# Optimization experiments

Hardware: AMD Instinct MI355X
Metric: run time of the kernel (lower is better)

## Reference

```python
import jax, jax.numpy as jnp
import numpy as np

N_CLASSES = 256
PER_CLASS = 128
N_SUPPORT = 5
N_QUERY = PER_CLASS - N_SUPPORT  # 123
N_VIEW = 2
D = 384
N = N_CLASSES * PER_CLASS  # 32768


def setup_inputs() -> dict:
    key = jax.random.key(0)
    k1, k2 = jax.random.split(key, 2)
    reps = jax.random.normal(k1, (N, N_VIEW, D), dtype=jnp.float32)
    # block-sorted labels: class c occupies rows [c*PER_CLASS, (c+1)*PER_CLASS)
    labels = (jnp.arange(N, dtype=jnp.int32) // PER_CLASS).astype(jnp.int32)
    return {"reps": reps, "labels": labels}


def reference(reps, labels):
    # labels are block-sorted per class, so the original's
    # labels.eq(c).nonzero()[:n_support] / [n_support:] gathers are static reshapes.
    reps_r = reps.reshape(N_CLASSES, PER_CLASS, N_VIEW, D)
    # class-mean prototypes over the support set: [C, V, D]
    prototypes = reps_r[:, :N_SUPPORT].mean(axis=1)
    # query samples: [C*N_QUERY, V, D]
    queries = reps_r[:, N_SUPPORT:].reshape(N_CLASSES * N_QUERY, N_VIEW, D)

    x2 = jnp.sum(queries * queries, axis=-1)            # [n, V]
    y2 = jnp.sum(prototypes * prototypes, axis=-1)      # [m, V]
    xy = jnp.einsum('nvd,mvd->nmv', queries, prototypes)  # [n, m, V]
    dists = x2[:, None, :] + y2[None, :, :] - 2.0 * xy

    # log_softmax over the prototype (class) axis
    log_p_y = jax.nn.log_softmax(-dists, axis=1)
    log_p_y = log_p_y.reshape(N_CLASSES, N_QUERY, N_CLASSES, N_VIEW)

    # gather the true-class log-prob for each query / view
    cls = jnp.arange(N_CLASSES)
    correct = log_p_y[cls, :, cls, :]  # [C, N_QUERY, V]
    loss = -correct.mean()
    return loss
```

## Files before the change

### kernel.cpp

```cpp
#include <hip/hip_runtime.h>
#include <hip/hip_bf16.h>
#include <math.h>

#define NCLS 256
#define PER_CLASS 128
#define NSUP 5
#define NQRY 123
#define NVIEW 2
#define DD 384
#define NQ_TOT (NCLS * NQRY)
#define BM 128
#define BK 32
#define QSTR 40
#define PSTR 40

#define PROTO_F (NVIEW * NCLS * DD)

typedef __attribute__((ext_vector_type(8))) short short8;
typedef __attribute__((ext_vector_type(4))) float floatx4;

union FragU { uint4 u; short8 s; };
union PkU { __hip_bfloat162 b2; unsigned int u; };

__device__ __forceinline__ unsigned int cvt2bf(float lo, float hi) {
    PkU p;
    p.b2 = __float22bfloat162_rn(make_float2(lo, hi));
    return p.u;
}

__global__ __launch_bounds__(256) void proto_kernel(const float* __restrict__ reps,
                                                    float* __restrict__ protof,
                                                    ushort* __restrict__ pbf) {
    int g = blockIdx.x * 256 + threadIdx.x;
    int d = g % DD;
    int rest = g / DD;
    int c = rest & (NCLS - 1);
    int v = rest >> 8;
    const float* p = reps + ((size_t)(c * PER_CLASS) * NVIEW + v) * DD + d;
    float s = 0.f;
#pragma unroll
    for (int k = 0; k < NSUP; ++k) s += p[(size_t)k * NVIEW * DD];
    s *= 0.2f;
    protof[g] = s;
    __hip_bfloat16 h = __float2bfloat16(s);
    pbf[g] = *reinterpret_cast<ushort*>(&h);
}

__global__ __launch_bounds__(64) void y2_kernel(const float* __restrict__ protof,
                                                float* __restrict__ y2) {
    int b = blockIdx.x;
    int lane = threadIdx.x;
    const float* p = protof + (size_t)b * DD;
    float s = 0.f;
#pragma unroll
    for (int k = 0; k < DD / 64; ++k) { float x = p[lane + 64 * k]; s += x * x; }
#pragma unroll
    for (int o = 1; o < 64; o <<= 1) s += __shfl_xor(s, o);
    if (lane == 0) y2[b] = s;
}

__global__ __launch_bounds__(256, 2) void main_kernel(const float* __restrict__ reps,
                                                      const ushort* __restrict__ pbf,
                                                      const float* __restrict__ y2g,
                                                      float* __restrict__ out) {
    __shared__ ushort q_lds[BM * QSTR];
    __shared__ ushort p_lds[NCLS * PSTR];
    __shared__ float pmx[BM][2];
    __shared__ float pse[BM][2];
    __shared__ float wred[8];

    const int t = threadIdx.x;
    const int v = blockIdx.y;
    const int q0 = blockIdx.x * BM;
    const int wave = t >> 6;
    const int lane = t & 63;
    const int col = lane & 15;
    const int quad = lane >> 4;
    const int wm = wave >> 1;
    const int wn = wave & 1;

    const int sqrow = t >> 1;
    const int sqh = (t & 1) * 16;
    const int nq = q0 + sqrow;
    const float* qsrc = reps +
        (size_t)((nq / NQRY) * PER_CLASS + NSUP + (nq % NQRY)) * (NVIEW * DD) + v * DD + sqh;
    const ushort* psrc = pbf + (size_t)(v * NCLS + t) * DD;

    floatx4 acc[4][8];
#pragma unroll
    for (int mt = 0; mt < 4; ++mt)
#pragma unroll
        for (int nt = 0; nt < 8; ++nt) acc[mt][nt] = (floatx4)0.f;

    for (int kt = 0; kt < DD / BK; ++kt) {
        float4 qf0 = *(const float4*)(qsrc + kt * BK);
        float4 qf1 = *(const float4*)(qsrc + kt * BK + 4);
        float4 qf2 = *(const float4*)(qsrc + kt * BK + 8);
        float4 qf3 = *(const float4*)(qsrc + kt * BK + 12);
        const uint4* pp = (const uint4*)(psrc + kt * BK);
        uint4 pl0 = pp[0], pl1 = pp[1], pl2 = pp[2], pl3 = pp[3];

        if (kt) __syncthreads();

        uint4 qw0, qw1;
        qw0.x = cvt2bf(qf0.x, qf0.y); qw0.y = cvt2bf(qf0.z, qf0.w);
        qw0.z = cvt2bf(qf1.x, qf1.y); qw0.w = cvt2bf(qf1.z, qf1.w);
        qw1.x = cvt2bf(qf2.x, qf2.y); qw1.y = cvt2bf(qf2.z, qf2.w);
        qw1.z = cvt2bf(qf3.x, qf3.y); qw1.w = cvt2bf(qf3.z, qf3.w);
        *(uint4*)&q_lds[sqrow * QSTR + sqh] = qw0;
        *(uint4*)&q_lds[sqrow * QSTR + sqh + 8] = qw1;
        *(uint4*)&p_lds[t * PSTR + 0] = pl0;
        *(uint4*)&p_lds[t * PSTR + 8] = pl1;
        *(uint4*)&p_lds[t * PSTR + 16] = pl2;
        *(uint4*)&p_lds[t * PSTR + 24] = pl3;
        __syncthreads();

        short8 af[4];
#pragma unroll
        for (int mt = 0; mt < 4; ++mt) {
            FragU f;
            f.u = *(const uint4*)&q_lds[(wm * 64 + mt * 16 + col) * QSTR + quad * 8];
            af[mt] = f.s;
        }
#pragma unroll
        for (int nt = 0; nt < 8; ++nt) {
            FragU b;
            b.u = *(const uint4*)&p_lds[(wn * 128 + nt * 16 + col) * PSTR + quad * 8];
#pragma unroll
            for (int mt = 0; mt < 4; ++mt)
                acc[mt][nt] = __builtin_amdgcn_mfma_f32_16x16x32_bf16(af[mt], b.s, acc[mt][nt], 0, 0, 0);
        }
    }

    float y2c[8];
#pragma unroll
    for (int nt = 0; nt < 8; ++nt) y2c[nt] = y2g[v * NCLS + wn * 128 + nt * 16 + col];

    float corr = 0.f;
#pragma unroll
    for (int mt = 0; mt < 4; ++mt) {
#pragma unroll
        for (int r = 0; r < 4; ++r) {
            const int qloc = wm * 64 + mt * 16 + quad * 4 + r;
            const int n = q0 + qloc;
            const int cn = n / NQRY;
            float s[8];
            float mx = -1e30f;
#pragma unroll
            for (int nt = 0; nt < 8; ++nt) {
                s[nt] = 2.f * acc[mt][nt][r] - y2c[nt];
                mx = fmaxf(mx, s[nt]);
                if (cn == wn * 128 + nt * 16 + col) corr += s[nt];
            }
#pragma unroll
            for (int o = 1; o < 16; o <<= 1) mx = fmaxf(mx, __shfl_xor(mx, o));
            float e = 0.f;
#pragma unroll
            for (int nt = 0; nt < 8; ++nt) e += __expf(s[nt] - mx);
#pragma unroll
            for (int o = 1; o < 16; o <<= 1) e += __shfl_xor(e, o);
            if (col == 0) { pmx[qloc][wn] = mx; pse[qloc][wn] = e; }
        }
    }
#pragma unroll
    for (int o = 1; o < 64; o <<= 1) corr += __shfl_xor(corr, o);
    if (lane == 0) wred[wave] = corr;
    __syncthreads();

    float lval = 0.f;
    if (t < BM) {
        float m0 = pmx[t][0], m1 = pmx[t][1];
        float M = fmaxf(m0, m1);
        float E = pse[t][0] * __expf(m0 - M) + pse[t][1] * __expf(m1 - M);
        lval = M + __logf(E);
    }
#pragma unroll
    for (int o = 1; o < 64; o <<= 1) lval += __shfl_xor(lval, o);
    if (lane == 0) wred[4 + wave] = lval;
    __syncthreads();

    if (t == 0) {
        float tot = (wred[4] + wred[5] + wred[6] + wred[7]) -
                    (wred[0] + wred[1] + wred[2] + wred[3]);
        atomicAdd(out, tot * (1.f / (float)(NQ_TOT * NVIEW)));
    }
}

extern "C" void kernel_launch(void* const* d_in, const int* in_sizes, int n_in,
                              void* d_out, int out_size, void* d_ws, size_t ws_size,
                              hipStream_t stream) {
    const float* reps = (const float*)d_in[0];
    float* ws = (float*)d_ws;
    float* protof = ws;
    float* y2 = ws + PROTO_F;
    ushort* pbf = (ushort*)(ws + PROTO_F + 512);
    float* out = (float*)d_out;

    hipMemsetAsync(out, 0, sizeof(float), stream);
    proto_kernel<<<dim3(PROTO_F / 256), dim3(256), 0, stream>>>(reps, protof, pbf);
    y2_kernel<<<dim3(NVIEW * NCLS), dim3(64), 0, stream>>>(protof, y2);
    main_kernel<<<dim3(NQ_TOT / BM, NVIEW), dim3(256), 0, stream>>>(reps, pbf, y2, out);
}
```

Measured before the change: 169.0 us.

## Load tiles directly to LDS via global_load_lds with XOR-swizzled layout

Replaces the register-staged global->LDS copies with direct global_load_lds 16-byte transfers for both query (fp32) and prototype (bf16) tiles. It uses XOR swizzles instead of row padding to avoid bank conflicts. The fp32->bf16 conversion of queries moves from the staging step to fragment load time, so each wave converts its own A fragments. This cuts register pressure and VALU staging work but doubles the LDS footprint for query tiles. It also drops the software overlap where global loads were issued before the barrier.

```diff
diff --git a/kernel.cpp b/kernel.cpp
--- a/kernel.cpp
+++ b/kernel.cpp
@@ -11,8 +11,6 @@
 #define NQ_TOT (NCLS * NQRY)
 #define BM 128
 #define BK 32
-#define QSTR 40
-#define PSTR 40
 
 #define PROTO_F (NVIEW * NCLS * DD)
 
@@ -26,6 +24,12 @@
     PkU p;
     p.b2 = __float22bfloat162_rn(make_float2(lo, hi));
     return p.u;
+}
+
+__device__ __forceinline__ void load16(const void* g, void* l) {
+    __builtin_amdgcn_global_load_lds(
+        (const __attribute__((address_space(1))) unsigned int*)g,
+        (__attribute__((address_space(3))) unsigned int*)l, 16, 0, 0);
 }
 
 __global__ __launch_bounds__(256) void proto_kernel(const float* __restrict__ reps,
@@ -63,8 +67,8 @@
                                                       const ushort* __restrict__ pbf,
                                                       const float* __restrict__ y2g,
                                                       float* __restrict__ out) {
-    __shared__ ushort q_lds[BM * QSTR];
-    __shared__ ushort p_lds[NCLS * PSTR];
+    __shared__ float q_lds[BM * BK];
+    __shared__ ushort p_lds[NCLS * BK];
     __shared__ float pmx[BM][2];
     __shared__ float pse[BM][2];
     __shared__ float wred[8];
@@ -79,12 +83,25 @@
     const int wm = wave >> 1;
     const int wn = wave & 1;
 
-    const int sqrow = t >> 1;
-    const int sqh = (t & 1) * 16;
-    const int nq = q0 + sqrow;
-    const float* qsrc = reps +
-        (size_t)((nq / NQRY) * PER_CLASS + NSUP + (nq % NQRY)) * (NVIEW * DD) + v * DD + sqh;
-    const ushort* psrc = pbf + (size_t)(v * NCLS + t) * DD;
+    const int l8 = lane >> 3, c8 = lane & 7;
+    const int cdq = c8 ^ l8;
+    const int l4 = lane >> 2;
+    const int cdp = (lane & 3) ^ ((lane >> 3) & 3);
+    const float* qptr[4];
+    const ushort* pptr[4];
+#pragma unroll
+    for (int i = 0; i < 4; ++i) {
+        int r = wave * 32 + i * 8 + l8;
+        int nq = q0 + r;
+        qptr[i] = reps + (size_t)((nq / NQRY) * PER_CLASS + NSUP + (nq % NQRY)) * (NVIEW * DD) +
+                  v * DD + cdq * 4;
+        int pr = wave * 64 + i * 16 + l4;
+        pptr[i] = pbf + (size_t)(v * NCLS + pr) * DD + cdp * 8;
+    }
+
+    const float* abase0 = q_lds + (wm * 64 + col) * 32 + ((2 * quad + 0) ^ (col & 7)) * 4;
+    const float* abase1 = q_lds + (wm * 64 + col) * 32 + ((2 * quad + 1) ^ (col & 7)) * 4;
+    const ushort* bbase = p_lds + (wn * 128 + col) * 32 + (quad ^ ((col >> 1) & 3)) * 8;
 
     floatx4 acc[4][8];
 #pragma unroll
@@ -93,39 +110,30 @@
         for (int nt = 0; nt < 8; ++nt) acc[mt][nt] = (floatx4)0.f;
 
     for (int kt = 0; kt < DD / BK; ++kt) {
-        float4 qf0 = *(const float4*)(qsrc + kt * BK);
-        float4 qf1 = *(const float4*)(qsrc + kt * BK + 4);
-        float4 qf2 = *(const float4*)(qsrc + kt * BK + 8);
-        float4 qf3 = *(const float4*)(qsrc + kt * BK + 12);
-        const uint4* pp = (const uint4*)(psrc + kt * BK);
-        uint4 pl0 = pp[0], pl1 = pp[1], pl2 = pp[2], pl3 = pp[3];
-
         if (kt) __syncthreads();
-
-        uint4 qw0, qw1;
-        qw0.x = cvt2bf(qf0.x, qf0.y); qw0.y = cvt2bf(qf0.z, qf0.w);
-        qw0.z = cvt2bf(qf1.x, qf1.y); qw0.w = cvt2bf(qf1.z, qf1.w);
-        qw1.x = cvt2bf(qf2.x, qf2.y); qw1.y = cvt2bf(qf2.z, qf2.w);
-        qw1.z = cvt2bf(qf3.x, qf3.y); qw1.w = cvt2bf(qf3.z, qf3.w);
-        *(uint4*)&q_lds[sqrow * QSTR + sqh] = qw0;
-        *(uint4*)&q_lds[sqrow * QSTR + sqh + 8] = qw1;
-        *(uint4*)&p_lds[t * PSTR + 0] = pl0;
-        *(uint4*)&p_lds[t * PSTR + 8] = pl1;
-        *(uint4*)&p_lds[t * PSTR + 16] = pl2;
-        *(uint4*)&p_lds[t * PSTR + 24] = pl3;
+#pragma unroll
+        for (int i = 0; i < 4; ++i) {
+            load16(qptr[i] + kt * BK, q_lds + (wave * 4 + i) * 256);
+            load16(pptr[i] + kt * BK, p_lds + (wave * 4 + i) * 512);
+        }
         __syncthreads();
 
         short8 af[4];
 #pragma unroll
         for (int mt = 0; mt < 4; ++mt) {
+            float4 a0 = *(const float4*)(abase0 + mt * 512);
+            float4 a1 = *(const float4*)(abase1 + mt * 512);
             FragU f;
-            f.u = *(const uint4*)&q_lds[(wm * 64 + mt * 16 + col) * QSTR + quad * 8];
+            f.u.x = cvt2bf(a0.x, a0.y);
+            f.u.y = cvt2bf(a0.z, a0.w);
+            f.u.z = cvt2bf(a1.x, a1.y);
+            f.u.w = cvt2bf(a1.z, a1.w);
             af[mt] = f.s;
         }
 #pragma unroll
         for (int nt = 0; nt < 8; ++nt) {
             FragU b;
-            b.u = *(const uint4*)&p_lds[(wn * 128 + nt * 16 + col) * PSTR + quad * 8];
+            b.u = *(const uint4*)(bbase + nt * 512);
 #pragma unroll
             for (int mt = 0; mt < 4; ++mt)
                 acc[mt][nt] = __builtin_amdgcn_mfma_f32_16x16x32_bf16(af[mt], b.s, acc[mt][nt], 0, 0, 0);
```

Result: no change. 168.3 us (-0.4%).

## Fuse prototype norm into proto kernel and double GEMM K-tile to 64

Applied to the files above, without the earlier changes.

Merges the prototype-mean and squared-norm kernels into one launch: each block handles one class/view row and reduces the squared norm with shuffles and shared memory, so the fp32 prototype buffer is no longer written and read back. The main GEMM kernel now uses a K-tile of 64 instead of 32, halving the number of barrier pairs and staging iterations, with two MFMA sub-steps per tile. The cost is about twice the LDS (padded stride 72) and more staging registers per iteration, which may reduce occupancy.

```diff
diff --git a/kernel.cpp b/kernel.cpp
--- a/kernel.cpp
+++ b/kernel.cpp
@@ -10,11 +10,8 @@
 #define DD 384
 #define NQ_TOT (NCLS * NQRY)
 #define BM 128
-#define BK 32
-#define QSTR 40
-#define PSTR 40
-
-#define PROTO_F (NVIEW * NCLS * DD)
+#define BK 64
+#define RSTR 72
 
 typedef __attribute__((ext_vector_type(8))) short short8;
 typedef __attribute__((ext_vector_type(4))) float floatx4;
@@ -28,43 +25,34 @@
     return p.u;
 }
 
-__global__ __launch_bounds__(256) void proto_kernel(const float* __restrict__ reps,
-                                                    float* __restrict__ protof,
-                                                    ushort* __restrict__ pbf) {
-    int g = blockIdx.x * 256 + threadIdx.x;
-    int d = g % DD;
-    int rest = g / DD;
-    int c = rest & (NCLS - 1);
-    int v = rest >> 8;
+__global__ __launch_bounds__(384) void proto_kernel(const float* __restrict__ reps,
+                                                    ushort* __restrict__ pbf,
+                                                    float* __restrict__ y2) {
+    __shared__ float wp[6];
+    const int b = blockIdx.x;
+    const int c = b & 255, v = b >> 8;
+    const int d = threadIdx.x;
     const float* p = reps + ((size_t)(c * PER_CLASS) * NVIEW + v) * DD + d;
     float s = 0.f;
 #pragma unroll
     for (int k = 0; k < NSUP; ++k) s += p[(size_t)k * NVIEW * DD];
     s *= 0.2f;
-    protof[g] = s;
     __hip_bfloat16 h = __float2bfloat16(s);
-    pbf[g] = *reinterpret_cast<ushort*>(&h);
-}
-
-__global__ __launch_bounds__(64) void y2_kernel(const float* __restrict__ protof,
-                                                float* __restrict__ y2) {
-    int b = blockIdx.x;
-    int lane = threadIdx.x;
-    const float* p = protof + (size_t)b * DD;
-    float s = 0.f;
+    pbf[(size_t)b * DD + d] = *reinterpret_cast<ushort*>(&h);
+    float q = s * s;
 #pragma unroll
-    for (int k = 0; k < DD / 64; ++k) { float x = p[lane + 64 * k]; s += x * x; }
-#pragma unroll
-    for (int o = 1; o < 64; o <<= 1) s += __shfl_xor(s, o);
-    if (lane == 0) y2[b] = s;
+    for (int o = 1; o < 64; o <<= 1) q += __shfl_xor(q, o);
+    if ((d & 63) == 0) wp[d >> 6] = q;
+    __syncthreads();
+    if (d == 0) y2[b] = wp[0] + wp[1] + wp[2] + wp[3] + wp[4] + wp[5];
 }
 
 __global__ __launch_bounds__(256, 2) void main_kernel(const float* __restrict__ reps,
                                                       const ushort* __restrict__ pbf,
                                                       const float* __restrict__ y2g,
                                                       float* __restrict__ out) {
-    __shared__ ushort q_lds[BM * QSTR];
-    __shared__ ushort p_lds[NCLS * PSTR];
+    __shared__ ushort q_lds[BM * RSTR];
+    __shared__ ushort p_lds[NCLS * RSTR];
     __shared__ float pmx[BM][2];
     __shared__ float pse[BM][2];
     __shared__ float wred[8];
@@ -79,12 +67,14 @@
     const int wm = wave >> 1;
     const int wn = wave & 1;
 
-    const int sqrow = t >> 1;
-    const int sqh = (t & 1) * 16;
-    const int nq = q0 + sqrow;
+    const int sq = t >> 1;
+    const int h = (t & 1) * 32;
+    const int nq = q0 + sq;
     const float* qsrc = reps +
-        (size_t)((nq / NQRY) * PER_CLASS + NSUP + (nq % NQRY)) * (NVIEW * DD) + v * DD + sqh;
+        (size_t)((nq / NQRY) * PER_CLASS + NSUP + (nq % NQRY)) * (NVIEW * DD) + v * DD + h;
     const ushort* psrc = pbf + (size_t)(v * NCLS + t) * DD;
+    ushort* qdst = &q_lds[sq * RSTR + h];
+    ushort* pdst = &p_lds[t * RSTR];
 
     floatx4 acc[4][8];
 #pragma unroll
@@ -93,42 +83,45 @@
         for (int nt = 0; nt < 8; ++nt) acc[mt][nt] = (floatx4)0.f;
 
     for (int kt = 0; kt < DD / BK; ++kt) {
-        float4 qf0 = *(const float4*)(qsrc + kt * BK);
-        float4 qf1 = *(const float4*)(qsrc + kt * BK + 4);
-        float4 qf2 = *(const float4*)(qsrc + kt * BK + 8);
-        float4 qf3 = *(const float4*)(qsrc + kt * BK + 12);
-        const uint4* pp = (const uint4*)(psrc + kt * BK);
-        uint4 pl0 = pp[0], pl1 = pp[1], pl2 = pp[2], pl3 = pp[3];
+        float4 qf[8];
+        uint4 pl[8];
+#pragma unroll
+        for (int i = 0; i < 8; ++i) qf[i] = *(const float4*)(qsrc + kt * BK + i * 4);
+#pragma unroll
+        for (int i = 0; i < 8; ++i) pl[i] = ((const uint4*)(psrc + kt * BK))[i];
+        uint4 qw[4];
+#pragma unroll
+        for (int i = 0; i < 4; ++i) {
+            qw[i].x = cvt2bf(qf[2 * i].x, qf[2 * i].y);
+            qw[i].y = cvt2bf(qf[2 * i].z, qf[2 * i].w);
+            qw[i].z = cvt2bf(qf[2 * i + 1].x, qf[2 * i + 1].y);
+            qw[i].w = cvt2bf(qf[2 * i + 1].z, qf[2 * i + 1].w);
+        }
 
         if (kt) __syncthreads();
-
-        uint4 qw0, qw1;
-        qw0.x = cvt2bf(qf0.x, qf0.y); qw0.y = cvt2bf(qf0.z, qf0.w);
-        qw0.z = cvt2bf(qf1.x, qf1.y); qw0.w = cvt2bf(qf1.z, qf1.w);
-        qw1.x = cvt2bf(qf2.x, qf2.y); qw1.y = cvt2bf(qf2.z, qf2.w);
-        qw1.z = cvt2bf(qf3.x, qf3.y); qw1.w = cvt2bf(qf3.z, qf3.w);
-        *(uint4*)&q_lds[sqrow * QSTR + sqh] = qw0;
-        *(uint4*)&q_lds[sqrow * QSTR + sqh + 8] = qw1;
-        *(uint4*)&p_lds[t * PSTR + 0] = pl0;
-        *(uint4*)&p_lds[t * PSTR + 8] = pl1;
-        *(uint4*)&p_lds[t * PSTR + 16] = pl2;
-        *(uint4*)&p_lds[t * PSTR + 24] = pl3;
+#pragma unroll
+        for (int i = 0; i < 4; ++i) *(uint4*)(qdst + h * 0 + i * 8) = qw[i];
+#pragma unroll
+        for (int i = 0; i < 8; ++i) *(uint4*)(pdst + i * 8) = pl[i];
         __syncthreads();
 
-        short8 af[4];
 #pragma unroll
-        for (int mt = 0; mt < 4; ++mt) {
-            FragU f;
-            f.u = *(const uint4*)&q_lds[(wm * 64 + mt * 16 + col) * QSTR + quad * 8];
-            af[mt] = f.s;
-        }
+        for (int ks = 0; ks < 2; ++ks) {
+            short8 af[4];
 #pragma unroll
-        for (int nt = 0; nt < 8; ++nt) {
-            FragU b;
-            b.u = *(const uint4*)&p_lds[(wn * 128 + nt * 16 + col) * PSTR + quad * 8];
+            for (int mt = 0; mt < 4; ++mt) {
+                FragU f;
+                f.u = *(const uint4*)&q_lds[(wm * 64 + mt * 16 + col) * RSTR + ks * 32 + quad * 8];
+                af[mt] = f.s;
+            }
 #pragma unroll
-            for (int mt = 0; mt < 4; ++mt)
-                acc[mt][nt] = __builtin_amdgcn_mfma_f32_16x16x32_bf16(af[mt], b.s, acc[mt][nt], 0, 0, 0);
+            for (int nt = 0; nt < 8; ++nt) {
+                FragU b;
+                b.u = *(const uint4*)&p_lds[(wn * 128 + nt * 16 + col) * RSTR + ks * 32 + quad * 8];
+#pragma unroll
+                for (int mt = 0; mt < 4; ++mt)
+                    acc[mt][nt] = __builtin_amdgcn_mfma_f32_16x16x32_bf16(af[mt], b.s, acc[mt][nt], 0, 0, 0);
+            }
         }
     }
 
@@ -191,13 +184,11 @@
                               hipStream_t stream) {
     const float* reps = (const float*)d_in[0];
     float* ws = (float*)d_ws;
-    float* protof = ws;
-    float* y2 = ws + PROTO_F;
-    ushort* pbf = (ushort*)(ws + PROTO_F + 512);
+    ushort* pbf = (ushort*)ws;
+    float* y2 = (float*)(pbf + NVIEW * NCLS * DD);
     float* out = (float*)d_out;
 
     hipMemsetAsync(out, 0, sizeof(float), stream);
-    proto_kernel<<<dim3(PROTO_F / 256), dim3(256), 0, stream>>>(reps, protof, pbf);
-    y2_kernel<<<dim3(NVIEW * NCLS), dim3(64), 0, stream>>>(protof, y2);
+    proto_kernel<<<dim3(NVIEW * NCLS), dim3(DD), 0, stream>>>(reps, pbf, y2);
     main_kernel<<<dim3(NQ_TOT / BM, NVIEW), dim3(256), 0, stream>>>(reps, pbf, y2, out);
 }
```

New measurement: 198.6 us. +17.5%, slower.
